# Performance work log

Measured on AMD Instinct MI355X. Metric: run time of the kernel, lower is better.

## Reference

```python
import jax, jax.numpy as jnp
import numpy as np

EPS = 1e-5  # haiku LayerNorm default
BIG = 1e9


def layernorm(x, scale, offset):
    mu = jnp.mean(x, axis=-1, keepdims=True)
    var = jnp.var(x, axis=-1, keepdims=True)
    return scale * (x - mu) * jax.lax.rsqrt(var + EPS) + offset


def setup_inputs() -> dict:
    key = jax.random.key(0)
    ks = iter(jax.random.split(key, 32))
    N_res, N_tok, C, H = 4096, 512, 384, 8
    kd = C // H  # 48, key_dim and value_dim per head
    F = 4 * C    # transition hidden
    s = 0.02
    inp = {
        "original": jax.random.normal(next(ks), (1, N_res, C), jnp.float32),
        "resampled": jax.random.normal(next(ks), (1, N_tok, C), jnp.float32),
        "attention_mask": (jax.random.uniform(next(ks), (H, N_tok, N_res)) < 0.9).astype(jnp.float32),
        "output_mask": jnp.ones((1, N_tok), jnp.float32),
        "input_mask": jnp.ones((1, N_res), jnp.float32),
        # cross-attention LayerNorms
        "qn_scale": jnp.ones((C,), jnp.float32), "qn_offset": jnp.zeros((C,), jnp.float32),
        "dn_scale": jnp.ones((C,), jnp.float32), "dn_offset": jnp.zeros((C,), jnp.float32),
        # attention projections
        "query_w": jax.random.normal(next(ks), (C, H, kd), jnp.float32) * s,
        "key_w": jax.random.normal(next(ks), (C, H, kd), jnp.float32) * s,
        "value_w": jax.random.normal(next(ks), (C, H, kd), jnp.float32) * s,
        "gating_w": jax.random.normal(next(ks), (C, H, kd), jnp.float32) * s,
        "gating_b": jnp.ones((H, kd), jnp.float32),
        "output_w": jax.random.normal(next(ks), (H, kd, C), jnp.float32) * s,
        "output_b": jnp.zeros((C,), jnp.float32),
        # resampled transition
        "rt_ln_scale": jnp.ones((C,), jnp.float32), "rt_ln_offset": jnp.zeros((C,), jnp.float32),
        "rt_w1": jax.random.normal(next(ks), (C, F), jnp.float32) * s, "rt_b1": jnp.zeros((F,), jnp.float32),
        "rt_w2": jax.random.normal(next(ks), (F, C), jnp.float32) * s, "rt_b2": jnp.zeros((C,), jnp.float32),
        # original transition
        "ot_ln_scale": jnp.ones((C,), jnp.float32), "ot_ln_offset": jnp.zeros((C,), jnp.float32),
        "ot_w1": jax.random.normal(next(ks), (C, F), jnp.float32) * s, "ot_b1": jnp.zeros((F,), jnp.float32),
        "ot_w2": jax.random.normal(next(ks), (F, C), jnp.float32) * s, "ot_b2": jnp.zeros((C,), jnp.float32),
    }
    return inp


def reference(original, resampled, attention_mask, output_mask, input_mask,
              qn_scale, qn_offset, dn_scale, dn_offset,
              query_w, key_w, value_w, gating_w, gating_b, output_w, output_b,
              rt_ln_scale, rt_ln_offset, rt_w1, rt_b1, rt_w2, rt_b2,
              ot_ln_scale, ot_ln_offset, ot_w1, ot_b1, ot_w2, ot_b2):
    # ---- CrossAttention (deterministic; dropout rate 0) ----
    bias = BIG * (attention_mask - 1.0)          # [H, T, R]
    q_in = layernorm(resampled, qn_scale, qn_offset)   # [1, T, C]
    d_in = layernorm(original, dn_scale, dn_offset)    # [1, R, C]
    kd = query_w.shape[-1]
    q = jnp.einsum('bqa,ahc->bqhc', q_in, query_w) * kd ** (-0.5)
    k = jnp.einsum('bka,ahc->bkhc', d_in, key_w)
    v = jnp.einsum('bka,ahc->bkhc', d_in, value_w)
    logits = jnp.einsum('bqhc,bkhc->bhqk', q, k) + bias[None]  # [1, H, T, R]
    weights = jax.nn.softmax(logits, axis=-1)
    weighted_avg = jnp.einsum('bhqk,bkhc->bqhc', weights, v)
    gate = jax.nn.sigmoid(jnp.einsum('bqc,chv->bqhv', q_in, gating_w) + gating_b)
    weighted_avg = weighted_avg * gate
    attn_out = jnp.einsum('bqhc,hco->bqo', weighted_avg, output_w) + output_b
    resampled = resampled + attn_out             # residual (dropout off)
    # ---- resampled Transition + residual ----
    t = layernorm(resampled, rt_ln_scale, rt_ln_offset)
    t = jax.nn.relu(t @ rt_w1 + rt_b1) @ rt_w2 + rt_b2
    resampled = resampled + t
    # ---- original Transition + residual ----
    t = layernorm(original, ot_ln_scale, ot_ln_offset)
    t = jax.nn.relu(t @ ot_w1 + ot_b1) @ ot_w2 + ot_b2
    original = original + t
    return resampled.astype(jnp.float32), original.astype(jnp.float32)
```

## Files before the change

### kernel.cpp

```cpp
#include <hip/hip_runtime.h>
#include <hip/hip_bf16.h>
#include <cstdint>

typedef unsigned short u16;
typedef __attribute__((ext_vector_type(8))) __bf16 bf16x8;
typedef __attribute__((ext_vector_type(4))) float f32x4;
typedef __attribute__((ext_vector_type(4))) short s16x4;
typedef __attribute__((ext_vector_type(4))) unsigned u32x4;

#define VSTR 4160

__device__ __forceinline__ u16 f2bf(float f) {
  union { float f; unsigned u; } v; v.f = f;
  unsigned r = (v.u + 0x7FFFu + ((v.u >> 16) & 1u)) >> 16;
  return (u16)r;
}

__device__ __forceinline__ void gll16(const u16* gp, u16* lp) {
  auto g1 = reinterpret_cast<const __attribute__((address_space(1))) void*>(
      reinterpret_cast<uintptr_t>(gp));
  auto l3 = reinterpret_cast<__attribute__((address_space(3))) void*>(
      reinterpret_cast<uintptr_t>(lp));
  __builtin_amdgcn_global_load_lds(g1, l3, 16, 0, 0);
}

__global__ __launch_bounds__(256) void mask_bits(const float* __restrict__ mask,
                                                 u16* __restrict__ mb) {
  const int t = blockIdx.x * 256 + threadIdx.x;
  const float* src = mask + (size_t)t * 16;
  unsigned b = 0;
#pragma unroll
  for (int j = 0; j < 4; ++j) {
    const f32x4 v = *(const f32x4*)(src + 4 * j);
#pragma unroll
    for (int k = 0; k < 4; ++k) b |= (v[k] != 0.f ? 1u : 0u) << (4 * j + k);
  }
  mb[t] = (u16)b;
}

__global__ __launch_bounds__(128) void ln_all(
    const float* __restrict__ orig, const float* __restrict__ resam,
    const float* __restrict__ dn_s, const float* __restrict__ dn_o, u16* __restrict__ dinb,
    const float* __restrict__ ot_s, const float* __restrict__ ot_o, u16* __restrict__ otin,
    const float* __restrict__ qn_s, const float* __restrict__ qn_o, u16* __restrict__ qin) {
  const int row = blockIdx.x;
  const int t = threadIdx.x;
  const bool isOrig = row < 4096;
  const float* xr = isOrig ? orig + (size_t)row * 384 : resam + (size_t)(row - 4096) * 384;
  float v0 = xr[t], v1 = xr[t + 128], v2 = xr[t + 256];
  float sum = v0 + v1 + v2;
  float sq = v0 * v0 + v1 * v1 + v2 * v2;
#pragma unroll
  for (int off = 32; off > 0; off >>= 1) {
    sum += __shfl_xor(sum, off);
    sq += __shfl_xor(sq, off);
  }
  __shared__ float red[4];
  if ((t & 63) == 0) { red[(t >> 6) * 2] = sum; red[(t >> 6) * 2 + 1] = sq; }
  __syncthreads();
  sum = red[0] + red[2];
  sq = red[1] + red[3];
  const float mu = sum * (1.f / 384.f);
  const float rstd = rsqrtf(sq * (1.f / 384.f) - mu * mu + 1e-5f);
#pragma unroll
  for (int j = 0; j < 3; ++j) {
    const int cc = t + 128 * j;
    const float xv = (j == 0 ? v0 : (j == 1 ? v1 : v2));
    const float xn = (xv - mu) * rstd;
    if (isOrig) {
      dinb[(size_t)row * 384 + cc] = f2bf(dn_s[cc] * xn + dn_o[cc]);
      otin[(size_t)row * 384 + cc] = f2bf(ot_s[cc] * xn + ot_o[cc]);
    } else {
      qin[(size_t)(row - 4096) * 384 + cc] = f2bf(qn_s[cc] * xn + qn_o[cc]);
    }
  }
}

__global__ __launch_bounds__(128) void ln_kernel(
    const float* __restrict__ x,
    const float* __restrict__ s1, const float* __restrict__ o1, u16* __restrict__ y1) {
  const int row = blockIdx.x;
  const int t = threadIdx.x;
  const float* xr = x + (size_t)row * 384;
  float v0 = xr[t], v1 = xr[t + 128], v2 = xr[t + 256];
  float sum = v0 + v1 + v2;
  float sq = v0 * v0 + v1 * v1 + v2 * v2;
#pragma unroll
  for (int off = 32; off > 0; off >>= 1) {
    sum += __shfl_xor(sum, off);
    sq += __shfl_xor(sq, off);
  }
  __shared__ float red[4];
  if ((t & 63) == 0) { red[(t >> 6) * 2] = sum; red[(t >> 6) * 2 + 1] = sq; }
  __syncthreads();
  sum = red[0] + red[2];
  sq = red[1] + red[3];
  const float mu = sum * (1.f / 384.f);
  const float rstd = rsqrtf(sq * (1.f / 384.f) - mu * mu + 1e-5f);
#pragma unroll
  for (int j = 0; j < 3; ++j) {
    const int cc = t + 128 * j;
    const float xv = (j == 0 ? v0 : (j == 1 ? v1 : v2));
    y1[(size_t)row * 384 + cc] = f2bf(s1[cc] * ((xv - mu) * rstd) + o1[cc]);
  }
}

struct TBatch {
  const float* in[9];
  u16* out[9];
  int K[9], N[9];
  float scale[9];
  int boff[10];
};

__global__ __launch_bounds__(256) void transpose_all(TBatch tb) {
  __shared__ float tile[32][33];
  const int bid = blockIdx.x;
  int j = 0;
  while (j < 8 && bid >= tb.boff[j + 1]) ++j;
  const int lb = bid - tb.boff[j];
  const int NB = tb.N[j] >> 5;
  const int bx = lb % NB, by = lb / NB;
  const float* in = tb.in[j];
  u16* out = tb.out[j];
  const int K = tb.K[j], N = tb.N[j];
  const float scale = tb.scale[j];
  const int tx = threadIdx.x, ty = threadIdx.y;
  const int nb = bx * 32, kb = by * 32;
#pragma unroll
  for (int i = 0; i < 4; ++i)
    tile[ty + 8 * i][tx] = in[(size_t)(kb + ty + 8 * i) * N + nb + tx];
  __syncthreads();
#pragma unroll
  for (int i = 0; i < 4; ++i)
    out[(size_t)(nb + ty + 8 * i) * K + kb + tx] = f2bf(tile[tx][ty + 8 * i] * scale);
}

struct GArgs {
  const u16* A; const u16* Bt;
  int M, N, K, Kld;
  const float* bias; const float* bias2; const float* residual;
  float* outf; u16* outb; u16* outb2;
};

template <int BM, int BN, int EPI>
__global__ __launch_bounds__(256, (BM == 128 ? 2 : 4)) void gemm_bt(GArgs g) {
  constexpr int MT = BM / 32, NT = BN / 32;
  const int tid = threadIdx.x;
  const int w = tid >> 6;
  const int lane = tid & 63;
  const int gq = lane >> 4, c = lane & 15;
  const int brow = blockIdx.y * BM, bcol = blockIdx.x * BN;
  const int wm = (w >> 1) * (BM / 2), wn = (w & 1) * (BN / 2);
  __shared__ u16 As[2][BM][64];
  __shared__ u16 Bs[2][BN][64];
  const int K = g.K;
  const int Kld = g.Kld;
  const size_t koff = (size_t)blockIdx.z * K;

  f32x4 acc[MT][NT];
#pragma unroll
  for (int mt = 0; mt < MT; ++mt)
#pragma unroll
    for (int nt = 0; nt < NT; ++nt)
#pragma unroll
      for (int r = 0; r < 4; ++r) acc[mt][nt][r] = 0.f;

  const int srow = lane >> 3;
  const int schunk = (lane & 7) ^ srow;
  const u16* aSrc = g.A + (size_t)(brow + w * (BM / 4) + srow) * Kld + koff + schunk * 8;
  const u16* bSrc = g.Bt + (size_t)(bcol + w * (BN / 4) + srow) * Kld + koff + schunk * 8;

  auto STAGE = [&](int buf, int k0) {
#pragma unroll
    for (int i = 0; i < BM / 32; ++i)
      gll16(aSrc + (size_t)(8 * i) * Kld + k0, &As[buf][w * (BM / 4) + i * 8][0]);
#pragma unroll
    for (int i = 0; i < BN / 32; ++i)
      gll16(bSrc + (size_t)(8 * i) * Kld + k0, &Bs[buf][w * (BN / 4) + i * 8][0]);
  };

  auto COMPUTE = [&](int buf) {
#pragma unroll
    for (int ks = 0; ks < 2; ++ks) {
      bf16x8 af[MT], bfv[NT];
#pragma unroll
      for (int mt = 0; mt < MT; ++mt) {
        const int row = wm + mt * 16 + c;
        const int ch = ((ks << 2) | gq) ^ (row & 7);
        af[mt] = *(const bf16x8*)&As[buf][row][ch * 8];
      }
#pragma unroll
      for (int nt = 0; nt < NT; ++nt) {
        const int row = wn + nt * 16 + c;
        const int ch = ((ks << 2) | gq) ^ (row & 7);
        bfv[nt] = *(const bf16x8*)&Bs[buf][row][ch * 8];
      }
#pragma unroll
      for (int mt = 0; mt < MT; ++mt)
#pragma unroll
        for (int nt = 0; nt < NT; ++nt)
          acc[mt][nt] =
              __builtin_amdgcn_mfma_f32_16x16x32_bf16(af[mt], bfv[nt], acc[mt][nt], 0, 0, 0);
    }
  };

  const int NTILES = K >> 6;
  STAGE(0, 0);
  __syncthreads();
  int cur = 0;
  for (int t = 0; t < NTILES; ++t) {
    if (t + 1 < NTILES) STAGE(cur ^ 1, (t + 1) << 6);
    COMPUTE(cur);
    __syncthreads();
    cur ^= 1;
  }

  const int N = g.N;
#pragma unroll
  for (int mt = 0; mt < MT; ++mt) {
#pragma unroll
    for (int nt = 0; nt < NT; ++nt) {
      const int n = bcol + wn + nt * 16 + c;
#pragma unroll
      for (int r = 0; r < 4; ++r) {
        const int m = brow + wm + mt * 16 + 4 * gq + r;
        const float v = acc[mt][nt][r];
        if (EPI == 0) {
          g.outb[(size_t)m * N + n] = f2bf(fmaxf(v + g.bias[n], 0.f));
        } else if (EPI == 1) {
          g.outf[(size_t)m * N + n] = v + g.bias[n] + g.residual[(size_t)m * N + n];
        } else if (EPI == 2) {
          if (n < 384)
            g.outb[(size_t)(n / 48) * 4096 * 64 + (size_t)m * 64 + (n % 48)] = f2bf(v);
          else
            g.outb2[(size_t)(n - 384) * VSTR + m] = f2bf(v);
        } else if (EPI == 3) {
          if (n < 384)
            g.outb[(size_t)(n / 48) * 512 * 64 + (size_t)m * 64 + (n % 48)] = f2bf(v);
          else {
            const float sg = v + g.bias2[n - 384];
            g.outf[(size_t)m * 384 + (n - 384)] = 1.f / (1.f + __expf(-sg));
          }
        } else {
          g.outf[(size_t)blockIdx.z * g.M * N + (size_t)m * N + n] = v;
        }
      }
    }
  }
}

__global__ __launch_bounds__(256, 2) void attn_kernel(
    const u16* __restrict__ Kh, const u16* __restrict__ Qb, const u16* __restrict__ Vt,
    const unsigned char* __restrict__ mbits, float* __restrict__ partO,
    float* __restrict__ partL) {
  const int tid = threadIdx.x;
  const int w = tid >> 6;
  const int lane = tid & 63;
  const int gq = lane >> 4, c = lane & 15;
  const int qg = blockIdx.x, h = blockIdx.y, z = blockIdx.z;
  const int qt = qg * 4 + w;
  const int kb = z * 512;

  __shared__ u16 Ks[2][128][64];
  __shared__ u16 Vs[2][48][128];

  const u16* qrow = Qb + ((size_t)h * 512 + qt * 16 + c) * 64;
  const bf16x8 qf0 = *(const bf16x8*)(qrow + 8 * gq);
  const bf16x8 qf1 = *(const bf16x8*)(qrow + 32 + 8 * gq);

  const unsigned char* mrow = mbits + ((size_t)h * 512 + qt * 16 + c) * 512 + z * 64;
  u32x4 mbAll[4];
#pragma unroll
  for (int ch = 0; ch < 4; ++ch) mbAll[ch] = *(const u32x4*)(mrow + ch * 16);

  const int krow8 = lane >> 3;
  const int kch = (lane & 7) ^ krow8;
  const u16* kbase = Kh + (size_t)h * 4096 * 64;
  const int vrow4 = lane >> 4;
  const int vk16 = lane & 15;

  auto STAGE = [&](int buf, int ch) {
    const int k0 = kb + ch * 128;
#pragma unroll
    for (int j = 0; j < 4; ++j) {
      const int row = w * 32 + j * 8 + krow8;
      gll16(kbase + (size_t)(k0 + row) * 64 + kch * 8, &Ks[buf][w * 32 + j * 8][0]);
    }
#pragma unroll
    for (int j = 0; j < 3; ++j) {
      const int d = w * 12 + j * 4 + vrow4;
      const int sk = vk16 ^ (d & 15);
      gll16(Vt + (size_t)(h * 48 + d) * VSTR + k0 + sk * 8, &Vs[buf][w * 12 + j * 4][0]);
    }
  };

  f32x4 O0, O1, O2;
#pragma unroll
  for (int r = 0; r < 4; ++r) { O0[r] = 0.f; O1[r] = 0.f; O2[r] = 0.f; }
  float psum = 0.f;
  f32x4 z4;
#pragma unroll
  for (int r = 0; r < 4; ++r) z4[r] = 0.f;

  STAGE(0, 0);
  __syncthreads();
  int cur = 0;
  for (int ch = 0; ch < 4; ++ch) {
    if (ch + 1 < 4) STAGE(cur ^ 1, ch + 1);
#pragma unroll
    for (int s = 0; s < 4; ++s) {
      const int keyA = s * 32 + c;
      const int keyB = keyA + 16;
      const bf16x8 kA0 = *(const bf16x8*)&Ks[cur][keyA][(gq ^ (keyA & 7)) * 8];
      const bf16x8 kA1 = *(const bf16x8*)&Ks[cur][keyA][((4 + gq) ^ (keyA & 7)) * 8];
      const bf16x8 kB0 = *(const bf16x8*)&Ks[cur][keyB][(gq ^ (keyB & 7)) * 8];
      const bf16x8 kB1 = *(const bf16x8*)&Ks[cur][keyB][((4 + gq) ^ (keyB & 7)) * 8];

      f32x4 s0 = __builtin_amdgcn_mfma_f32_16x16x32_bf16(kA0, qf0, z4, 0, 0, 0);
      s0 = __builtin_amdgcn_mfma_f32_16x16x32_bf16(kA1, qf1, s0, 0, 0, 0);
      f32x4 s1 = __builtin_amdgcn_mfma_f32_16x16x32_bf16(kB0, qf0, z4, 0, 0, 0);
      s1 = __builtin_amdgcn_mfma_f32_16x16x32_bf16(kB1, qf1, s1, 0, 0, 0);

      const unsigned word = mbAll[ch][s];
      const unsigned wd0 = word >> (4 * gq);
      const unsigned wd1 = word >> (16 + 4 * gq);
      float p0[4], p1[4];
#pragma unroll
      for (int r = 0; r < 4; ++r) {
        p0[r] = ((wd0 >> r) & 1u) ? __expf(s0[r]) : 0.f;
        p1[r] = ((wd1 >> r) & 1u) ? __expf(s1[r]) : 0.f;
        psum += p0[r] + p1[r];
      }
      s16x4 pa0, pa1;
      ((unsigned*)&pa0)[0] = __builtin_amdgcn_perm(__builtin_bit_cast(unsigned, p0[1]),
                                                   __builtin_bit_cast(unsigned, p0[0]), 0x07060302u);
      ((unsigned*)&pa0)[1] = __builtin_amdgcn_perm(__builtin_bit_cast(unsigned, p0[3]),
                                                   __builtin_bit_cast(unsigned, p0[2]), 0x07060302u);
      ((unsigned*)&pa1)[0] = __builtin_amdgcn_perm(__builtin_bit_cast(unsigned, p1[1]),
                                                   __builtin_bit_cast(unsigned, p1[0]), 0x07060302u);
      ((unsigned*)&pa1)[1] = __builtin_amdgcn_perm(__builtin_bit_cast(unsigned, p1[3]),
                                                   __builtin_bit_cast(unsigned, p1[2]), 0x07060302u);

#pragma unroll
      for (int nt = 0; nt < 3; ++nt) {
        const int row = nt * 16 + c;
        const int klA = s * 32 + 4 * gq;
        const int klB = klA + 16;
        const s16x4 vfA = *(const s16x4*)&Vs[cur][row][(((klA >> 3) ^ c) << 3) + (gq & 1) * 4];
        const s16x4 vfB = *(const s16x4*)&Vs[cur][row][(((klB >> 3) ^ c) << 3) + (gq & 1) * 4];
        f32x4& O = (nt == 0 ? O0 : (nt == 1 ? O1 : O2));
        O = __builtin_amdgcn_mfma_f32_16x16x16bf16_1k(pa0, vfA, O, 0, 0, 0);
        O = __builtin_amdgcn_mfma_f32_16x16x16bf16_1k(pa1, vfB, O, 0, 0, 0);
      }
    }
    __syncthreads();
    cur ^= 1;
  }

  psum += __shfl_xor(psum, 16);
  psum += __shfl_xor(psum, 32);

  float* pO = partO + (((size_t)z * 32 + qt) * 8 + h) * 768;
#pragma unroll
  for (int r = 0; r < 4; ++r) {
    const int q = 4 * gq + r;
    pO[q * 48 + c] = O0[r];
    pO[q * 48 + 16 + c] = O1[r];
    pO[q * 48 + 32 + c] = O2[r];
  }
  if (gq == 0)
    partL[(((size_t)z * 32 + qt) * 8 + h) * 16 + c] = psum;
}

__global__ __launch_bounds__(256) void attn_merge(
    const float* __restrict__ partO, const float* __restrict__ partL,
    const float* __restrict__ gate, u16* __restrict__ attng) {
  const int qt = blockIdx.x, h = blockIdx.y;
  for (int idx = threadIdx.x; idx < 768; idx += 256) {
    const int q = idx / 48, d = idx % 48;
    float O = 0.f, L = 0.f;
#pragma unroll
    for (int z = 0; z < 8; ++z) {
      O += partO[(((size_t)z * 32 + qt) * 8 + h) * 768 + idx];
      L += partL[(((size_t)z * 32 + qt) * 8 + h) * 16 + q];
    }
    const size_t off = (size_t)(qt * 16 + q) * 384 + h * 48 + d;
    attng[off] = f2bf(O / L * gate[off]);
  }
}

__global__ __launch_bounds__(256) void merge_res(
    const float* __restrict__ pT1, const float* __restrict__ res2,
    const float* __restrict__ rtb2, float* __restrict__ out_res) {
  const int i = blockIdx.x * 256 + threadIdx.x;
  const int n0 = (i * 4) % 384;
  f32x4 v = *(const f32x4*)(res2 + (size_t)i * 4);
#pragma unroll
  for (int z = 0; z < 4; ++z) {
    const f32x4 pz = *(const f32x4*)(pT1 + (size_t)z * 512 * 384 + (size_t)i * 4);
#pragma unroll
    for (int r = 0; r < 4; ++r) v[r] += pz[r];
  }
  const f32x4 b = *(const f32x4*)(rtb2 + n0);
#pragma unroll
  for (int r = 0; r < 4; ++r) v[r] += b[r];
  *(f32x4*)(out_res + (size_t)i * 4) = v;
}

extern "C" void kernel_launch(void* const* d_in, const int* in_sizes, int n_in,
                              void* d_out, int out_size, void* d_ws, size_t ws_size,
                              hipStream_t stream) {
  (void)in_sizes; (void)n_in; (void)out_size; (void)ws_size;
  const float* original = (const float*)d_in[0];
  const float* resampled = (const float*)d_in[1];
  const float* amask = (const float*)d_in[2];
  const float* qn_s = (const float*)d_in[5];
  const float* qn_o = (const float*)d_in[6];
  const float* dn_s = (const float*)d_in[7];
  const float* dn_o = (const float*)d_in[8];
  const float* w_q = (const float*)d_in[9];
  const float* w_k = (const float*)d_in[10];
  const float* w_v = (const float*)d_in[11];
  const float* w_g = (const float*)d_in[12];
  const float* b_g = (const float*)d_in[13];
  const float* w_o = (const float*)d_in[14];
  const float* b_o = (const float*)d_in[15];
  const float* rt_s = (const float*)d_in[16];
  const float* rt_o = (const float*)d_in[17];
  const float* rtw1 = (const float*)d_in[18];
  const float* rtb1 = (const float*)d_in[19];
  const float* rtw2 = (const float*)d_in[20];
  const float* rtb2 = (const float*)d_in[21];
  const float* ot_s = (const float*)d_in[22];
  const float* ot_o = (const float*)d_in[23];
  const float* otw1 = (const float*)d_in[24];
  const float* otb1 = (const float*)d_in[25];
  const float* otw2 = (const float*)d_in[26];
  const float* otb2 = (const float*)d_in[27];

  float* out_res = (float*)d_out;
  float* out_orig = out_res + 512 * 384;

  char* p = (char*)d_ws;
  auto alloc = [&](size_t n) {
    void* r = (void*)p;
    p += (n + 255) & ~(size_t)255;
    return r;
  };
  u16* Kh = (u16*)alloc((size_t)8 * 4096 * 64 * 2);
  u16* Qb = (u16*)alloc((size_t)8 * 512 * 64 * 2);
  u16* dinb = (u16*)alloc(4096 * 384 * 2);
  u16* otin = (u16*)alloc(4096 * 384 * 2);
  u16* qin = (u16*)alloc(512 * 384 * 2);
  u16* Vt = (u16*)alloc((size_t)384 * VSTR * 2);
  float* gateb = (float*)alloc(512 * 384 * 4);
  u16* attng = (u16*)alloc(512 * 384 * 2);
  float* res2 = (float*)alloc(512 * 384 * 4);
  u16* tin = (u16*)alloc(512 * 384 * 2);
  u16* H1 = (u16*)alloc(512 * 1536 * 2);
  u16* H2 = (u16*)alloc((size_t)4096 * 1536 * 2);
  float* partT1 = (float*)alloc((size_t)4 * 512 * 384 * 4);
  float* partO = (float*)alloc((size_t)8 * 32 * 8 * 768 * 4);
  float* partL = (float*)alloc((size_t)8 * 32 * 8 * 16 * 4);
  u16* mbitsB = (u16*)alloc((size_t)8 * 512 * 512);
  u16* BtKV = (u16*)alloc(768 * 384 * 2);
  u16* BtQG = (u16*)alloc(768 * 384 * 2);
  u16* OwT = (u16*)alloc(384 * 384 * 2);
  u16* Rt1T = (u16*)alloc(1536 * 384 * 2);
  u16* Rt2T = (u16*)alloc(384 * 1536 * 2);
  u16* Ot1T = (u16*)alloc(1536 * 384 * 2);
  u16* Ot2T = (u16*)alloc(384 * 1536 * 2);

  hipMemsetAsync(Kh, 0, (size_t)8 * 4096 * 64 * 2 + (size_t)8 * 512 * 64 * 2, stream);

  mask_bits<<<4096, 256, 0, stream>>>(amask, mbitsB);

  {
    TBatch tb{};
    const float qscale = 0.14433756729740643f;
    const float* ins[9] = {w_q, w_g, w_k, w_v, w_o, rtw1, rtw2, otw1, otw2};
    u16* outs[9] = {BtQG, BtQG + 384 * 384, BtKV, BtKV + 384 * 384, OwT,
                    Rt1T, Rt2T, Ot1T, Ot2T};
    const int Ks[9] = {384, 384, 384, 384, 384, 384, 1536, 384, 1536};
    const int Ns[9] = {384, 384, 384, 384, 384, 1536, 384, 1536, 384};
    int off = 0;
    for (int j = 0; j < 9; ++j) {
      tb.in[j] = ins[j]; tb.out[j] = outs[j];
      tb.K[j] = Ks[j]; tb.N[j] = Ns[j];
      tb.scale[j] = (j == 0) ? qscale : 1.f;
      tb.boff[j] = off;
      off += (Ns[j] >> 5) * (Ks[j] >> 5);
    }
    tb.boff[9] = off;
    transpose_all<<<off, dim3(32, 8), 0, stream>>>(tb);
  }

  ln_all<<<4608, 128, 0, stream>>>(original, resampled, dn_s, dn_o, dinb,
                                   ot_s, ot_o, otin, qn_s, qn_o, qin);

  {
    GArgs a{};
    a.A = dinb; a.Bt = BtKV; a.M = 4096; a.N = 768; a.K = 384; a.Kld = 384;
    a.outb = Kh; a.outb2 = Vt;
    gemm_bt<128, 64, 2><<<dim3(12, 32), 256, 0, stream>>>(a);
  }
  {
    GArgs a{};
    a.A = qin; a.Bt = BtQG; a.M = 512; a.N = 768; a.K = 384; a.Kld = 384;
    a.outb = Qb; a.outf = gateb; a.bias2 = b_g;
    gemm_bt<64, 64, 3><<<dim3(12, 8), 256, 0, stream>>>(a);
  }

  attn_kernel<<<dim3(8, 8, 8), 256, 0, stream>>>(
      Kh, Qb, Vt, (const unsigned char*)mbitsB, partO, partL);
  attn_merge<<<dim3(32, 8), 256, 0, stream>>>(partO, partL, gateb, attng);

  {
    GArgs a{};
    a.A = attng; a.Bt = OwT; a.M = 512; a.N = 384; a.K = 384; a.Kld = 384;
    a.bias = b_o; a.residual = resampled; a.outf = res2;
    gemm_bt<64, 64, 1><<<dim3(6, 8), 256, 0, stream>>>(a);
  }
  ln_kernel<<<512, 128, 0, stream>>>(res2, rt_s, rt_o, tin);
  {
    GArgs a{};
    a.A = tin; a.Bt = Rt1T; a.M = 512; a.N = 1536; a.K = 384; a.Kld = 384;
    a.bias = rtb1; a.outb = H1;
    gemm_bt<64, 64, 0><<<dim3(24, 8), 256, 0, stream>>>(a);
  }
  {
    GArgs a{};
    a.A = H1; a.Bt = Rt2T; a.M = 512; a.N = 384; a.K = 384; a.Kld = 1536;
    a.outf = partT1;
    gemm_bt<64, 64, 4><<<dim3(6, 8, 4), 256, 0, stream>>>(a);
  }
  {
    GArgs a{};
    a.A = otin; a.Bt = Ot1T; a.M = 4096; a.N = 1536; a.K = 384; a.Kld = 384;
    a.bias = otb1; a.outb = H2;
    gemm_bt<128, 64, 0><<<dim3(24, 32), 256, 0, stream>>>(a);
  }
  {
    GArgs a{};
    a.A = H2; a.Bt = Ot2T; a.M = 4096; a.N = 384; a.K = 1536; a.Kld = 1536;
    a.bias = otb2; a.residual = original; a.outf = out_orig;
    gemm_bt<64, 64, 1><<<dim3(6, 64), 256, 0, stream>>>(a);
  }
  merge_res<<<192, 256, 0, stream>>>(partT1, res2, rtb2, out_res);
}
```

Measured before the change: 261.3 us.

## Fuse prep kernels, merge KV/QG GEMMs, and use atomic split-K epilogues

```diff
diff --git a/kernel.cpp b/kernel.cpp
--- a/kernel.cpp
+++ b/kernel.cpp
@@ -24,86 +24,13 @@
   __builtin_amdgcn_global_load_lds(g1, l3, 16, 0, 0);
 }
 
-__global__ __launch_bounds__(256) void mask_bits(const float* __restrict__ mask,
-                                                 u16* __restrict__ mb) {
-  const int t = blockIdx.x * 256 + threadIdx.x;
-  const float* src = mask + (size_t)t * 16;
-  unsigned b = 0;
-#pragma unroll
-  for (int j = 0; j < 4; ++j) {
-    const f32x4 v = *(const f32x4*)(src + 4 * j);
-#pragma unroll
-    for (int k = 0; k < 4; ++k) b |= (v[k] != 0.f ? 1u : 0u) << (4 * j + k);
-  }
-  mb[t] = (u16)b;
-}
-
-__global__ __launch_bounds__(128) void ln_all(
-    const float* __restrict__ orig, const float* __restrict__ resam,
-    const float* __restrict__ dn_s, const float* __restrict__ dn_o, u16* __restrict__ dinb,
-    const float* __restrict__ ot_s, const float* __restrict__ ot_o, u16* __restrict__ otin,
-    const float* __restrict__ qn_s, const float* __restrict__ qn_o, u16* __restrict__ qin) {
-  const int row = blockIdx.x;
-  const int t = threadIdx.x;
-  const bool isOrig = row < 4096;
-  const float* xr = isOrig ? orig + (size_t)row * 384 : resam + (size_t)(row - 4096) * 384;
-  float v0 = xr[t], v1 = xr[t + 128], v2 = xr[t + 256];
-  float sum = v0 + v1 + v2;
-  float sq = v0 * v0 + v1 * v1 + v2 * v2;
-#pragma unroll
-  for (int off = 32; off > 0; off >>= 1) {
-    sum += __shfl_xor(sum, off);
-    sq += __shfl_xor(sq, off);
-  }
-  __shared__ float red[4];
-  if ((t & 63) == 0) { red[(t >> 6) * 2] = sum; red[(t >> 6) * 2 + 1] = sq; }
-  __syncthreads();
-  sum = red[0] + red[2];
-  sq = red[1] + red[3];
-  const float mu = sum * (1.f / 384.f);
-  const float rstd = rsqrtf(sq * (1.f / 384.f) - mu * mu + 1e-5f);
-#pragma unroll
-  for (int j = 0; j < 3; ++j) {
-    const int cc = t + 128 * j;
-    const float xv = (j == 0 ? v0 : (j == 1 ? v1 : v2));
-    const float xn = (xv - mu) * rstd;
-    if (isOrig) {
-      dinb[(size_t)row * 384 + cc] = f2bf(dn_s[cc] * xn + dn_o[cc]);
-      otin[(size_t)row * 384 + cc] = f2bf(ot_s[cc] * xn + ot_o[cc]);
-    } else {
-      qin[(size_t)(row - 4096) * 384 + cc] = f2bf(qn_s[cc] * xn + qn_o[cc]);
-    }
-  }
-}
-
-__global__ __launch_bounds__(128) void ln_kernel(
-    const float* __restrict__ x,
-    const float* __restrict__ s1, const float* __restrict__ o1, u16* __restrict__ y1) {
-  const int row = blockIdx.x;
-  const int t = threadIdx.x;
-  const float* xr = x + (size_t)row * 384;
-  float v0 = xr[t], v1 = xr[t + 128], v2 = xr[t + 256];
-  float sum = v0 + v1 + v2;
-  float sq = v0 * v0 + v1 * v1 + v2 * v2;
-#pragma unroll
-  for (int off = 32; off > 0; off >>= 1) {
-    sum += __shfl_xor(sum, off);
-    sq += __shfl_xor(sq, off);
-  }
-  __shared__ float red[4];
-  if ((t & 63) == 0) { red[(t >> 6) * 2] = sum; red[(t >> 6) * 2 + 1] = sq; }
-  __syncthreads();
-  sum = red[0] + red[2];
-  sq = red[1] + red[3];
-  const float mu = sum * (1.f / 384.f);
-  const float rstd = rsqrtf(sq * (1.f / 384.f) - mu * mu + 1e-5f);
-#pragma unroll
-  for (int j = 0; j < 3; ++j) {
-    const int cc = t + 128 * j;
-    const float xv = (j == 0 ? v0 : (j == 1 ? v1 : v2));
-    y1[(size_t)row * 384 + cc] = f2bf(s1[cc] * ((xv - mu) * rstd) + o1[cc]);
-  }
-}
+#define PREP_B0 4096
+#define PREP_B1 6400
+#define PREP_B2 9424
+#define PREP_B3 9680
+#define PREP_B4 9712
+#define PREP_B5 9904
+#define PREP_B6 11440
 
 struct TBatch {
   const float* in[9];
@@ -113,38 +40,165 @@
   int boff[10];
 };
 
-__global__ __launch_bounds__(256) void transpose_all(TBatch tb) {
+struct PrepArgs {
+  const float* mask; u16* mb;
+  const float* orig; const float* resam;
+  const float* dn_s; const float* dn_o; u16* dinb;
+  const float* ot_s; const float* ot_o; u16* otin;
+  const float* qn_s; const float* qn_o; u16* qin;
+  TBatch tb;
+  u16* Kh; u16* Qb;
+  const float* b_o; float* res2;
+  const float* otb2; float* out_orig;
+};
+
+__global__ __launch_bounds__(256) void prep_kernel(PrepArgs a) {
+  const int bid = blockIdx.x;
+  const int tid = threadIdx.x;
   __shared__ float tile[32][33];
-  const int bid = blockIdx.x;
-  int j = 0;
-  while (j < 8 && bid >= tb.boff[j + 1]) ++j;
-  const int lb = bid - tb.boff[j];
-  const int NB = tb.N[j] >> 5;
-  const int bx = lb % NB, by = lb / NB;
-  const float* in = tb.in[j];
-  u16* out = tb.out[j];
-  const int K = tb.K[j], N = tb.N[j];
-  const float scale = tb.scale[j];
-  const int tx = threadIdx.x, ty = threadIdx.y;
-  const int nb = bx * 32, kb = by * 32;
-#pragma unroll
-  for (int i = 0; i < 4; ++i)
-    tile[ty + 8 * i][tx] = in[(size_t)(kb + ty + 8 * i) * N + nb + tx];
+  __shared__ float red[2][2][2];
+
+  if (bid < PREP_B0) {
+    const int t = bid * 256 + tid;
+    const float* src = a.mask + (size_t)t * 16;
+    unsigned b = 0;
+#pragma unroll
+    for (int j = 0; j < 4; ++j) {
+      const f32x4 v = *(const f32x4*)(src + 4 * j);
+#pragma unroll
+      for (int k = 0; k < 4; ++k) b |= (v[k] != 0.f ? 1u : 0u) << (4 * j + k);
+    }
+    a.mb[t] = (u16)b;
+  } else if (bid < PREP_B1) {
+    const int lb = bid - PREP_B0;
+    const int sub = tid >> 7;
+    const int t = tid & 127;
+    const int row = lb * 2 + sub;
+    const bool isOrig = row < 4096;
+    const float* xr = isOrig ? a.orig + (size_t)row * 384
+                             : a.resam + (size_t)(row - 4096) * 384;
+    float v0 = xr[t], v1 = xr[t + 128], v2 = xr[t + 256];
+    float sum = v0 + v1 + v2;
+    float sq = v0 * v0 + v1 * v1 + v2 * v2;
+#pragma unroll
+    for (int off = 32; off > 0; off >>= 1) {
+      sum += __shfl_xor(sum, off);
+      sq += __shfl_xor(sq, off);
+    }
+    if ((tid & 63) == 0) {
+      red[sub][(tid >> 6) & 1][0] = sum;
+      red[sub][(tid >> 6) & 1][1] = sq;
+    }
+    __syncthreads();
+    sum = red[sub][0][0] + red[sub][1][0];
+    sq = red[sub][0][1] + red[sub][1][1];
+    const float mu = sum * (1.f / 384.f);
+    const float rstd = rsqrtf(sq * (1.f / 384.f) - mu * mu + 1e-5f);
+#pragma unroll
+    for (int j = 0; j < 3; ++j) {
+      const int cc = t + 128 * j;
+      const float xv = (j == 0 ? v0 : (j == 1 ? v1 : v2));
+      const float xn = (xv - mu) * rstd;
+      if (isOrig) {
+        a.dinb[(size_t)row * 384 + cc] = f2bf(a.dn_s[cc] * xn + a.dn_o[cc]);
+        a.otin[(size_t)row * 384 + cc] = f2bf(a.ot_s[cc] * xn + a.ot_o[cc]);
+      } else {
+        a.qin[(size_t)(row - 4096) * 384 + cc] = f2bf(a.qn_s[cc] * xn + a.qn_o[cc]);
+      }
+    }
+  } else if (bid < PREP_B2) {
+    const int b = bid - PREP_B1;
+    int j = 0;
+    while (j < 8 && b >= a.tb.boff[j + 1]) ++j;
+    const int lb = b - a.tb.boff[j];
+    const int NB = a.tb.N[j] >> 5;
+    const int bx = lb % NB, by = lb / NB;
+    const float* in = a.tb.in[j];
+    u16* out = a.tb.out[j];
+    const int K = a.tb.K[j], N = a.tb.N[j];
+    const float scale = a.tb.scale[j];
+    const int tx = tid & 31, ty = tid >> 5;
+    const int nb = bx * 32, kb = by * 32;
+#pragma unroll
+    for (int i = 0; i < 4; ++i)
+      tile[ty + 8 * i][tx] = in[(size_t)(kb + ty + 8 * i) * N + nb + tx];
+    __syncthreads();
+#pragma unroll
+    for (int i = 0; i < 4; ++i)
+      out[(size_t)(nb + ty + 8 * i) * K + kb + tx] = f2bf(tile[tx][ty + 8 * i] * scale);
+  } else if (bid < PREP_B3) {
+    const int gi = (bid - PREP_B2) * 256 + tid;
+    const int r = gi >> 1, half = gi & 1;
+    u32x4 z{0u, 0u, 0u, 0u};
+    *(u32x4*)(a.Kh + (size_t)r * 64 + 48 + half * 8) = z;
+  } else if (bid < PREP_B4) {
+    const int gi = (bid - PREP_B3) * 256 + tid;
+    const int r = gi >> 1, half = gi & 1;
+    u32x4 z{0u, 0u, 0u, 0u};
+    *(u32x4*)(a.Qb + (size_t)r * 64 + 48 + half * 8) = z;
+  } else if (bid < PREP_B5) {
+    const int i = (bid - PREP_B4) * 256 + tid;
+    const int n0 = (i * 4) % 384;
+    f32x4 v = *(const f32x4*)(a.resam + (size_t)i * 4);
+    const f32x4 b = *(const f32x4*)(a.b_o + n0);
+#pragma unroll
+    for (int r = 0; r < 4; ++r) v[r] += b[r];
+    *(f32x4*)(a.res2 + (size_t)i * 4) = v;
+  } else {
+    const int i = (bid - PREP_B5) * 256 + tid;
+    const int n0 = (i * 4) % 384;
+    f32x4 v = *(const f32x4*)(a.orig + (size_t)i * 4);
+    const f32x4 b = *(const f32x4*)(a.otb2 + n0);
+#pragma unroll
+    for (int r = 0; r < 4; ++r) v[r] += b[r];
+    *(f32x4*)(a.out_orig + (size_t)i * 4) = v;
+  }
+}
+
+__global__ __launch_bounds__(256) void ln_rt(
+    const float* __restrict__ res2, const float* __restrict__ s1,
+    const float* __restrict__ o1, const float* __restrict__ rtb2,
+    u16* __restrict__ tin, float* __restrict__ out_res) {
+  const int sub = threadIdx.x >> 7;
+  const int t = threadIdx.x & 127;
+  const int row = blockIdx.x * 2 + sub;
+  __shared__ float red[2][2][2];
+  const float* xr = res2 + (size_t)row * 384;
+  float v0 = xr[t], v1 = xr[t + 128], v2 = xr[t + 256];
+  float sum = v0 + v1 + v2;
+  float sq = v0 * v0 + v1 * v1 + v2 * v2;
+#pragma unroll
+  for (int off = 32; off > 0; off >>= 1) {
+    sum += __shfl_xor(sum, off);
+    sq += __shfl_xor(sq, off);
+  }
+  if ((threadIdx.x & 63) == 0) {
+    red[sub][(threadIdx.x >> 6) & 1][0] = sum;
+    red[sub][(threadIdx.x >> 6) & 1][1] = sq;
+  }
   __syncthreads();
-#pragma unroll
-  for (int i = 0; i < 4; ++i)
-    out[(size_t)(nb + ty + 8 * i) * K + kb + tx] = f2bf(tile[tx][ty + 8 * i] * scale);
+  sum = red[sub][0][0] + red[sub][1][0];
+  sq = red[sub][0][1] + red[sub][1][1];
+  const float mu = sum * (1.f / 384.f);
+  const float rstd = rsqrtf(sq * (1.f / 384.f) - mu * mu + 1e-5f);
+#pragma unroll
+  for (int j = 0; j < 3; ++j) {
+    const int cc = t + 128 * j;
+    const float xv = (j == 0 ? v0 : (j == 1 ? v1 : v2));
+    tin[(size_t)row * 384 + cc] = f2bf(s1[cc] * ((xv - mu) * rstd) + o1[cc]);
+    out_res[(size_t)row * 384 + cc] = xv + rtb2[cc];
+  }
 }
 
 struct GArgs {
-  const u16* A; const u16* Bt;
+  const u16* A; const u16* Bt; const u16* Bt2;
   int M, N, K, Kld;
-  const float* bias; const float* bias2; const float* residual;
-  float* outf; u16* outb; u16* outb2;
+  const float* bias; const float* bias2;
+  float* outf; u16* outb; u16* outb2; u16* outb3;
 };
 
 template <int BM, int BN, int EPI>
-__global__ __launch_bounds__(256, (BM == 128 ? 2 : 4)) void gemm_bt(GArgs g) {
+__global__ __launch_bounds__(256, (BM == 128 ? 3 : 4)) void gemm_bt(GArgs g) {
   constexpr int MT = BM / 32, NT = BN / 32;
   const int tid = threadIdx.x;
   const int w = tid >> 6;
@@ -157,6 +211,7 @@
   const int K = g.K;
   const int Kld = g.Kld;
   const size_t koff = (size_t)blockIdx.z * K;
+  const u16* BT = (EPI == 7 && blockIdx.y >= 32) ? g.Bt2 : g.Bt;
 
   f32x4 acc[MT][NT];
 #pragma unroll
@@ -169,7 +224,7 @@
   const int srow = lane >> 3;
   const int schunk = (lane & 7) ^ srow;
   const u16* aSrc = g.A + (size_t)(brow + w * (BM / 4) + srow) * Kld + koff + schunk * 8;
-  const u16* bSrc = g.Bt + (size_t)(bcol + w * (BN / 4) + srow) * Kld + koff + schunk * 8;
+  const u16* bSrc = BT + (size_t)(bcol + w * (BN / 4) + srow) * Kld + koff + schunk * 8;
 
   auto STAGE = [&](int buf, int k0) {
 #pragma unroll
@@ -228,22 +283,23 @@
         const float v = acc[mt][nt][r];
         if (EPI == 0) {
           g.outb[(size_t)m * N + n] = f2bf(fmaxf(v + g.bias[n], 0.f));
-        } else if (EPI == 1) {
-          g.outf[(size_t)m * N + n] = v + g.bias[n] + g.residual[(size_t)m * N + n];
-        } else if (EPI == 2) {
-          if (n < 384)
-            g.outb[(size_t)(n / 48) * 4096 * 64 + (size_t)m * 64 + (n % 48)] = f2bf(v);
-          else
-            g.outb2[(size_t)(n - 384) * VSTR + m] = f2bf(v);
-        } else if (EPI == 3) {
-          if (n < 384)
-            g.outb[(size_t)(n / 48) * 512 * 64 + (size_t)m * 64 + (n % 48)] = f2bf(v);
-          else {
-            const float sg = v + g.bias2[n - 384];
-            g.outf[(size_t)m * 384 + (n - 384)] = 1.f / (1.f + __expf(-sg));
+        } else if (EPI == 5) {
+          atomicAdd(g.outf + (size_t)m * N + n, v);
+        } else if (EPI == 7) {
+          if (m < 4096) {
+            if (n < 384)
+              g.outb[(size_t)(n / 48) * 4096 * 64 + (size_t)m * 64 + (n % 48)] = f2bf(v);
+            else
+              g.outb2[(size_t)(n - 384) * VSTR + m] = f2bf(v);
+          } else {
+            const int mq = m - 4096;
+            if (n < 384)
+              g.outb3[(size_t)(n / 48) * 512 * 64 + (size_t)mq * 64 + (n % 48)] = f2bf(v);
+            else {
+              const float sg = v + g.bias2[n - 384];
+              g.outf[(size_t)mq * 384 + (n - 384)] = 1.f / (1.f + __expf(-sg));
+            }
           }
-        } else {
-          g.outf[(size_t)blockIdx.z * g.M * N + (size_t)m * N + n] = v;
         }
       }
     }
@@ -284,8 +340,8 @@
     const int k0 = kb + ch * 128;
 #pragma unroll
     for (int j = 0; j < 4; ++j) {
-      const int row = w * 32 + j * 8 + krow8;
-      gll16(kbase + (size_t)(k0 + row) * 64 + kch * 8, &Ks[buf][w * 32 + j * 8][0]);
+      gll16(kbase + (size_t)(k0 + w * 32 + j * 8 + krow8) * 64 + kch * 8,
+            &Ks[buf][w * 32 + j * 8][0]);
     }
 #pragma unroll
     for (int j = 0; j < 3; ++j) {
@@ -388,24 +444,6 @@
     const size_t off = (size_t)(qt * 16 + q) * 384 + h * 48 + d;
     attng[off] = f2bf(O / L * gate[off]);
   }
-}
-
-__global__ __launch_bounds__(256) void merge_res(
-    const float* __restrict__ pT1, const float* __restrict__ res2,
-    const float* __restrict__ rtb2, float* __restrict__ out_res) {
-  const int i = blockIdx.x * 256 + threadIdx.x;
-  const int n0 = (i * 4) % 384;
-  f32x4 v = *(const f32x4*)(res2 + (size_t)i * 4);
-#pragma unroll
-  for (int z = 0; z < 4; ++z) {
-    const f32x4 pz = *(const f32x4*)(pT1 + (size_t)z * 512 * 384 + (size_t)i * 4);
-#pragma unroll
-    for (int r = 0; r < 4; ++r) v[r] += pz[r];
-  }
-  const f32x4 b = *(const f32x4*)(rtb2 + n0);
-#pragma unroll
-  for (int r = 0; r < 4; ++r) v[r] += b[r];
-  *(f32x4*)(out_res + (size_t)i * 4) = v;
 }
 
 extern "C" void kernel_launch(void* const* d_in, const int* in_sizes, int n_in,
@@ -451,8 +489,8 @@
   u16* Kh = (u16*)alloc((size_t)8 * 4096 * 64 * 2);
   u16* Qb = (u16*)alloc((size_t)8 * 512 * 64 * 2);
   u16* dinb = (u16*)alloc(4096 * 384 * 2);
+  u16* qin = (u16*)alloc(512 * 384 * 2);
   u16* otin = (u16*)alloc(4096 * 384 * 2);
-  u16* qin = (u16*)alloc(512 * 384 * 2);
   u16* Vt = (u16*)alloc((size_t)384 * VSTR * 2);
   float* gateb = (float*)alloc(512 * 384 * 4);
   u16* attng = (u16*)alloc(512 * 384 * 2);
@@ -460,7 +498,6 @@
   u16* tin = (u16*)alloc(512 * 384 * 2);
   u16* H1 = (u16*)alloc(512 * 1536 * 2);
   u16* H2 = (u16*)alloc((size_t)4096 * 1536 * 2);
-  float* partT1 = (float*)alloc((size_t)4 * 512 * 384 * 4);
   float* partO = (float*)alloc((size_t)8 * 32 * 8 * 768 * 4);
   float* partL = (float*)alloc((size_t)8 * 32 * 8 * 16 * 4);
   u16* mbitsB = (u16*)alloc((size_t)8 * 512 * 512);
@@ -472,12 +509,13 @@
   u16* Ot1T = (u16*)alloc(1536 * 384 * 2);
   u16* Ot2T = (u16*)alloc(384 * 1536 * 2);
 
-  hipMemsetAsync(Kh, 0, (size_t)8 * 4096 * 64 * 2 + (size_t)8 * 512 * 64 * 2, stream);
-
-  mask_bits<<<4096, 256, 0, stream>>>(amask, mbitsB);
-
-  {
-    TBatch tb{};
+  {
+    PrepArgs pa{};
+    pa.mask = amask; pa.mb = mbitsB;
+    pa.orig = original; pa.resam = resampled;
+    pa.dn_s = dn_s; pa.dn_o = dn_o; pa.dinb = dinb;
+    pa.ot_s = ot_s; pa.ot_o = ot_o; pa.otin = otin;
+    pa.qn_s = qn_s; pa.qn_o = qn_o; pa.qin = qin;
     const float qscale = 0.14433756729740643f;
     const float* ins[9] = {w_q, w_g, w_k, w_v, w_o, rtw1, rtw2, otw1, otw2};
     u16* outs[9] = {BtQG, BtQG + 384 * 384, BtKV, BtKV + 384 * 384, OwT,
@@ -486,30 +524,25 @@
     const int Ns[9] = {384, 384, 384, 384, 384, 1536, 384, 1536, 384};
     int off = 0;
     for (int j = 0; j < 9; ++j) {
-      tb.in[j] = ins[j]; tb.out[j] = outs[j];
-      tb.K[j] = Ks[j]; tb.N[j] = Ns[j];
-      tb.scale[j] = (j == 0) ? qscale : 1.f;
-      tb.boff[j] = off;
+      pa.tb.in[j] = ins[j]; pa.tb.out[j] = outs[j];
+      pa.tb.K[j] = Ks[j]; pa.tb.N[j] = Ns[j];
+      pa.tb.scale[j] = (j == 0) ? qscale : 1.f;
+      pa.tb.boff[j] = off;
       off += (Ns[j] >> 5) * (Ks[j] >> 5);
     }
-    tb.boff[9] = off;
-    transpose_all<<<off, dim3(32, 8), 0, stream>>>(tb);
-  }
-
-  ln_all<<<4608, 128, 0, stream>>>(original, resampled, dn_s, dn_o, dinb,
-                                   ot_s, ot_o, otin, qn_s, qn_o, qin);
+    pa.tb.boff[9] = off;
+    pa.Kh = Kh; pa.Qb = Qb;
+    pa.b_o = b_o; pa.res2 = res2;
+    pa.otb2 = otb2; pa.out_orig = out_orig;
+    prep_kernel<<<PREP_B6, 256, 0, stream>>>(pa);
+  }
 
   {
     GArgs a{};
-    a.A = dinb; a.Bt = BtKV; a.M = 4096; a.N = 768; a.K = 384; a.Kld = 384;
-    a.outb = Kh; a.outb2 = Vt;
-    gemm_bt<128, 64, 2><<<dim3(12, 32), 256, 0, stream>>>(a);
-  }
-  {
-    GArgs a{};
-    a.A = qin; a.Bt = BtQG; a.M = 512; a.N = 768; a.K = 384; a.Kld = 384;
-    a.outb = Qb; a.outf = gateb; a.bias2 = b_g;
-    gemm_bt<64, 64, 3><<<dim3(12, 8), 256, 0, stream>>>(a);
+    a.A = dinb; a.Bt = BtKV; a.Bt2 = BtQG;
+    a.M = 4608; a.N = 768; a.K = 384; a.Kld = 384;
+    a.outb = Kh; a.outb2 = Vt; a.outb3 = Qb; a.outf = gateb; a.bias2 = b_g;
+    gemm_bt<128, 64, 7><<<dim3(12, 36), 256, 0, stream>>>(a);
   }
 
   attn_kernel<<<dim3(8, 8, 8), 256, 0, stream>>>(
@@ -518,11 +551,11 @@
 
   {
     GArgs a{};
-    a.A = attng; a.Bt = OwT; a.M = 512; a.N = 384; a.K = 384; a.Kld = 384;
-    a.bias = b_o; a.residual = resampled; a.outf = res2;
-    gemm_bt<64, 64, 1><<<dim3(6, 8), 256, 0, stream>>>(a);
-  }
-  ln_kernel<<<512, 128, 0, stream>>>(res2, rt_s, rt_o, tin);
+    a.A = attng; a.Bt = OwT; a.M = 512; a.N = 384; a.K = 128; a.Kld = 384;
+    a.outf = res2;
+    gemm_bt<64, 64, 5><<<dim3(6, 8, 3), 256, 0, stream>>>(a);
+  }
+  ln_rt<<<256, 256, 0, stream>>>(res2, rt_s, rt_o, rtb2, tin, out_res);
   {
     GArgs a{};
     a.A = tin; a.Bt = Rt1T; a.M = 512; a.N = 1536; a.K = 384; a.Kld = 384;
@@ -532,8 +565,8 @@
   {
     GArgs a{};
     a.A = H1; a.Bt = Rt2T; a.M = 512; a.N = 384; a.K = 384; a.Kld = 1536;
-    a.outf = partT1;
-    gemm_bt<64, 64, 4><<<dim3(6, 8, 4), 256, 0, stream>>>(a);
+    a.outf = out_res;
+    gemm_bt<64, 64, 5><<<dim3(6, 8, 4), 256, 0, stream>>>(a);
   }
   {
     GArgs a{};
@@ -543,9 +576,8 @@
   }
   {
     GArgs a{};
-    a.A = H2; a.Bt = Ot2T; a.M = 4096; a.N = 384; a.K = 1536; a.Kld = 1536;
-    a.bias = otb2; a.residual = original; a.outf = out_orig;
-    gemm_bt<64, 64, 1><<<dim3(6, 64), 256, 0, stream>>>(a);
-  }
-  merge_res<<<192, 256, 0, stream>>>(partT1, res2, rtb2, out_res);
-}
+    a.A = H2; a.Bt = Ot2T; a.M = 4096; a.N = 384; a.K = 768; a.Kld = 1536;
+    a.outf = out_orig;
+    gemm_bt<128, 64, 5><<<dim3(6, 32, 2), 256, 0, stream>>>(a);
+  }
+}
```

Result: faster. 245.0 us (-6.2%).
